# Performance work log

Measured on AMD Instinct MI355X. Metric: run time of the kernel, lower is better.

## Reference

```python
import jax, jax.numpy as jnp
import numpy as np
from jax import lax

BN_EPS = 1e-5
HEADS = 2


def dw_conv(x, w, stride, pad):
    # depthwise conv, NCHW, weight OIHW with I=1, groups=C
    return lax.conv_general_dilated(
        x, w, (stride, stride), [(pad, pad), (pad, pad)],
        dimension_numbers=('NCHW', 'OIHW', 'NCHW'),
        feature_group_count=x.shape[1])


def bn(x, g, b, m, v):
    inv = g * lax.rsqrt(v + BN_EPS)
    return (x - m[:, None, None]) * inv[:, None, None] + b[:, None, None]


def conv1x1(x, w, b):
    return jnp.einsum('bchw,oc->bohw', x, w) + b[:, None, None]


def setup_inputs() -> dict:
    key = jax.random.key(0)
    ks = jax.random.split(key, 20)
    B, C, H, W = 32, 128, 56, 56
    r = lambda i, shape, s=0.05: jax.random.normal(ks[i], shape, jnp.float32) * s
    return {
        'x': jax.random.normal(ks[0], (B, C, H, W), jnp.float32),
        'q_w': r(1, (C, C)), 'q_b': r(2, (C,)),
        'kv_w': r(3, (2 * C, C)), 'kv_b': r(4, (2 * C,)),
        'sr1_w': r(5, (C, 1, 4, 4), 0.2),
        'sr1_g': jax.random.uniform(ks[6], (C,), jnp.float32) + 0.5,
        'sr1_b': r(7, (C,)),
        'sr1_m': r(8, (C,)),
        'sr1_v': jax.random.uniform(ks[9], (C,), jnp.float32) + 0.5,
        'sr2_w': r(10, (C, 1, 1, 1), 0.5),
        'sr2_g': jax.random.uniform(ks[11], (C,), jnp.float32) + 0.5,
        'sr2_b': r(12, (C,)),
        'sr2_m': r(13, (C,)),
        'sr2_v': jax.random.uniform(ks[14], (C,), jnp.float32) + 0.5,
        'local_w': r(15, (C, 1, 3, 3), 0.2), 'local_b': r(16, (C,)),
    }


def reference(x, q_w, q_b, kv_w, kv_b,
              sr1_w, sr1_g, sr1_b, sr1_m, sr1_v,
              sr2_w, sr2_g, sr2_b, sr2_m, sr2_v,
              local_w, local_b):
    B, C, H, W = x.shape
    h = HEADS
    d = C // h
    scale = d ** -0.5

    # q projection: 1x1 conv -> [B, h, N, d]
    q = conv1x1(x, q_w, q_b)
    q = q.reshape(B, h, d, H * W).transpose(0, 1, 3, 2)

    # spatial reduction: depthwise strided conv + BN + ReLU, then depthwise 1x1 + BN
    kv = jax.nn.relu(bn(dw_conv(x, sr1_w, 4, 2), sr1_g, sr1_b, sr1_m, sr1_v))
    kv = bn(kv * sr2_w.reshape(C, 1, 1), sr2_g, sr2_b, sr2_m, sr2_v)

    # depthwise 3x3 local conv + residual
    kv = dw_conv(kv, local_w, 1, 1) + local_b[:, None, None] + kv

    # kv projection and split
    kvp = conv1x1(kv, kv_w, kv_b)
    k, v = jnp.split(kvp, 2, axis=1)
    Nk = k.shape[2] * k.shape[3]
    k = k.reshape(B, h, d, Nk)                       # [B,h,d,Nk]
    v = v.reshape(B, h, d, Nk).transpose(0, 1, 3, 2)  # [B,h,Nk,d]

    attn = jax.nn.softmax(jnp.einsum('bhnd,bhdm->bhnm', q, k) * scale, axis=-1)
    out = jnp.einsum('bhnm,bhmd->bhnd', attn, v)      # [B,h,N,d]
    return out.transpose(0, 1, 3, 2).reshape(B, C, H, W)
```

## Files before the change

### kernel.cpp

```cpp
#include <hip/hip_runtime.h>
#include <hip/hip_bf16.h>

#define B_    32
#define C_    128
#define H_    56
#define W_    56
#define N_    3136
#define HK_   15
#define NK_   225
#define D_    64
#define SCL_  0.1803368801111731f

typedef __attribute__((ext_vector_type(8))) short bf16x8;
typedef __attribute__((ext_vector_type(4))) float f32x4;

__device__ __forceinline__ float b2f(unsigned short u) {
    union { float f; unsigned int i; } x;
    x.i = ((unsigned int)u) << 16;
    return x.f;
}
__device__ __forceinline__ unsigned short f2b(float f) {
    __hip_bfloat16 h = __float2bfloat16(f);
    return *(unsigned short*)&h;
}
__device__ __forceinline__ unsigned int cvtpk(float a, float b) {
    unsigned int r;
    asm("v_cvt_pk_bf16_f32 %0, %1, %2" : "=v"(r) : "v"(a), "v"(b));
    return r;
}
__device__ __forceinline__ float exp2a(float x) {
    float r;
    asm("v_exp_f32 %0, %1" : "=v"(r) : "v"(x));
    return r;
}

__device__ __forceinline__ void gll16(const char* g, char* l) {
    __builtin_amdgcn_global_load_lds(
        (const __attribute__((address_space(1))) unsigned int*)g,
        (__attribute__((address_space(3))) unsigned int*)l,
        16, 0, 0);
}

__global__ __launch_bounds__(256) void prep_kernel(
        const float* __restrict__ x,
        const float* __restrict__ sr1_w, const float* __restrict__ sr1_g,
        const float* __restrict__ sr1_b, const float* __restrict__ sr1_m,
        const float* __restrict__ sr1_v, const float* __restrict__ sr2_w,
        const float* __restrict__ sr2_g, const float* __restrict__ sr2_b,
        const float* __restrict__ sr2_m, const float* __restrict__ sr2_v,
        const float* __restrict__ local_w, const float* __restrict__ local_b,
        const float* __restrict__ q_w, const float* __restrict__ q_b,
        const float* __restrict__ kv_w, const float* __restrict__ kv_b,
        float* __restrict__ kv2,
        unsigned short* __restrict__ wkq_sw, unsigned short* __restrict__ wv_sw,
        float* __restrict__ kwb, float* __restrict__ wb, float* __restrict__ qkb) {
    int tid = threadIdx.x;
    __shared__ float kvt[HK_][HK_ + 1];
    __shared__ float wq[64][16];

    if (blockIdx.x >= (unsigned)(B_ * C_)) {
        int bx = blockIdx.x - B_ * C_;
        int h  = bx >> 3, cg = bx & 7;
        for (int idx = tid; idx < 64 * 16; idx += 256)
            wq[idx >> 4][idx & 15] =
                q_w[(size_t)(h * 64 + (idx >> 4)) * 128 + cg * 16 + (idx & 15)];
        __syncthreads();
        {
            int cl = tid >> 4;
            int c  = cg * 16 + cl;
            int cp0 = (tid & 15) * 8;
            float acc[8];
#pragma unroll
            for (int i = 0; i < 8; ++i) acc[i] = 0.f;
            for (int e = 0; e < 64; ++e) {
                float wqv = wq[e][cl];
                const float* wkrow = kv_w + (size_t)(h * 64 + e) * 128 + cp0;
#pragma unroll
                for (int i = 0; i < 8; ++i) acc[i] += wqv * wkrow[i];
            }
            char* base = (char*)wkq_sw + (size_t)h * 32768 + (size_t)c * 256;
            ushort4 u0, u1;
            u0.x = f2b(acc[0] * SCL_); u0.y = f2b(acc[1] * SCL_);
            u0.z = f2b(acc[2] * SCL_); u0.w = f2b(acc[3] * SCL_);
            u1.x = f2b(acc[4] * SCL_); u1.y = f2b(acc[5] * SCL_);
            u1.z = f2b(acc[6] * SCL_); u1.w = f2b(acc[7] * SCL_);
            int sw = (c & 7) << 4;
            *(ushort4*)(base + ((cp0 * 2) ^ sw)) = u0;
            *(ushort4*)(base + ((cp0 * 2 + 8) ^ sw)) = u1;
        }
        if (tid < 16) {
            int cl = tid, c = cg * 16 + cl;
            float s = 0.f;
            for (int e = 0; e < 64; ++e) s += kv_b[h * 64 + e] * wq[e][cl];
            kwb[h * 128 + c] = s * SCL_;
        }
        if (cg == 0) {
            if (tid < 128) {
                float s = 0.f;
                for (int e = 0; e < 64; ++e)
                    s += q_b[h * 64 + e] * kv_w[(size_t)(h * 64 + e) * 128 + tid];
                wb[h * 128 + tid] = s * SCL_;
            }
            if (tid == 0) {
                float s = 0.f;
                for (int e = 0; e < 64; ++e) s += q_b[h * 64 + e] * kv_b[h * 64 + e];
                qkb[h] = s * SCL_;
            }
        }
        if (cg == 1) {
            for (int idx = tid; idx < 64 * 128; idx += 256) {
                int e = idx >> 7, cp = idx & 127;
                unsigned short val = f2b(kv_w[(size_t)(128 + h * 64 + e) * 128 + cp]);
                *(unsigned short*)((char*)wv_sw + (size_t)h * 16384 + (size_t)e * 256 +
                                   (((cp * 2) ^ ((e & 7) << 4)))) = val;
            }
        }
        return;
    }

    int bc = blockIdx.x;
    int c  = bc & (C_ - 1);
    const float* xp = x + (size_t)bc * (H_ * W_);
    int p = tid;
    int oy = p / HK_, ox = p % HK_;
    if (p < NK_) {
        float s = 0.f;
#pragma unroll
        for (int ky = 0; ky < 4; ++ky) {
            int iy = oy * 4 - 2 + ky;
            if (iy < 0 || iy >= H_) continue;
#pragma unroll
            for (int kx = 0; kx < 4; ++kx) {
                int ix = ox * 4 - 2 + kx;
                if (ix < 0 || ix >= W_) continue;
                s += xp[iy * W_ + ix] * sr1_w[c * 16 + ky * 4 + kx];
            }
        }
        float inv1 = sr1_g[c] * rsqrtf(sr1_v[c] + 1e-5f);
        s = (s - sr1_m[c]) * inv1 + sr1_b[c];
        s = fmaxf(s, 0.f);
        s *= sr2_w[c];
        float inv2 = sr2_g[c] * rsqrtf(sr2_v[c] + 1e-5f);
        s = (s - sr2_m[c]) * inv2 + sr2_b[c];
        kvt[oy][ox] = s;
    }
    __syncthreads();
    if (p < NK_) {
        float v = kvt[oy][ox] + local_b[c];
#pragma unroll
        for (int dy = -1; dy <= 1; ++dy) {
            int yy = oy + dy;
            if (yy < 0 || yy >= HK_) continue;
#pragma unroll
            for (int dx = -1; dx <= 1; ++dx) {
                int xx = ox + dx;
                if (xx < 0 || xx >= HK_) continue;
                v += kvt[yy][xx] * local_w[c * 9 + (dy + 1) * 3 + (dx + 1)];
            }
        }
        kv2[(size_t)bc * NK_ + p] = v;
    }
}

#define L2B(r, cb) ((r) * 256 + ((cb) ^ (((r) & 7) << 4)))
__global__ __launch_bounds__(256, 2) void kvw_kernel(
        const float* __restrict__ kv2,
        const float* __restrict__ kv_b,
        const unsigned short* __restrict__ wkq_sw,
        const unsigned short* __restrict__ wv_sw,
        const float* __restrict__ kwb,
        const float* __restrict__ wb,
        const float* __restrict__ qkb,
        unsigned short* __restrict__ kw,
        float* __restrict__ bias_s,
        unsigned short* __restrict__ vbuf) {
    int b = blockIdx.x, h = blockIdx.y, mh = blockIdx.z;
    int bh = b * 2 + h;
    int m0 = mh * 64;
    int tid = threadIdx.x;
    int lo = tid & 15, hi = (tid >> 4) & 3, wid = tid >> 6;

    __shared__ char K2[16384];
    __shared__ char WQ[32768];
    __shared__ char WV[16384];

    {
        const char* srcQ = (const char*)wkq_sw + (size_t)h * 32768 + tid * 16;
        char* dstQ = WQ + wid * 1024;
#pragma unroll
        for (int i = 0; i < 8; ++i) gll16(srcQ + i * 4096, dstQ + i * 4096);
        const char* srcV = (const char*)wv_sw + (size_t)h * 16384 + tid * 16;
        char* dstV = WV + wid * 1024;
#pragma unroll
        for (int i = 0; i < 4; ++i) gll16(srcV + i * 4096, dstV + i * 4096);
    }
    {
        int j = tid & 63;
        int mg = m0 + j;
        bool val = (mg < NK_);
#pragma unroll
        for (int it = 0; it < 8; ++it) {
            int c0 = (tid >> 6) * 4 + it * 16;
            ushort4 u;
            if (val) {
                const float* kp = kv2 + ((size_t)b * 128 + c0) * NK_ + mg;
                u.x = f2b(kp[0]);
                u.y = f2b(kp[NK_]);
                u.z = f2b(kp[2 * NK_]);
                u.w = f2b(kp[3 * NK_]);
            } else { u.x = 0; u.y = 0; u.z = 0; u.w = 0; }
            *(ushort4*)(K2 + L2B(j, c0 * 2)) = u;
        }
    }
    __syncthreads();

    bf16x8 aq[4];
#pragma unroll
    for (int ks = 0; ks < 4; ++ks)
        aq[ks] = *(const bf16x8*)(K2 + L2B(wid * 16 + lo, ks * 64 + hi * 16));

    char* kwB = (char*)kw + (size_t)bh * 65536;
#pragma unroll
    for (int ct = 0; ct < 8; ++ct) {
        f32x4 acc = {0.f, 0.f, 0.f, 0.f};
#pragma unroll
        for (int ks = 0; ks < 4; ++ks) {
            bf16x8 bq = *(const bf16x8*)(WQ + L2B(ct * 16 + lo, ks * 64 + hi * 16));
            acc = __builtin_amdgcn_mfma_f32_16x16x32_bf16(aq[ks], bq, acc, 0, 0, 0);
        }
        int c = ct * 16 + lo;
        float kb = kwb[h * 128 + c];
#pragma unroll
        for (int r = 0; r < 4; ++r) {
            int mg = m0 + wid * 16 + hi * 4 + r;
            *(unsigned short*)(kwB + (size_t)mg * 256 + (((c * 2) ^ ((mg & 7) << 4)))) =
                f2b(acc[r] + kb);
        }
    }

    char* vB = (char*)vbuf + (size_t)bh * 32768;
#pragma unroll
    for (int et = 0; et < 4; ++et) {
        f32x4 acc = {0.f, 0.f, 0.f, 0.f};
#pragma unroll
        for (int ks = 0; ks < 4; ++ks) {
            bf16x8 bv = *(const bf16x8*)(WV + L2B(et * 16 + lo, ks * 64 + hi * 16));
            acc = __builtin_amdgcn_mfma_f32_16x16x32_bf16(aq[ks], bv, acc, 0, 0, 0);
        }
        int e = et * 16 + lo;
        float vb = kv_b[128 + h * 64 + e];
#pragma unroll
        for (int r = 0; r < 4; ++r) {
            int mg = m0 + wid * 16 + hi * 4 + r;
            *(unsigned short*)(vB + (size_t)e * 512 + (((mg * 2) ^ ((e & 7) << 4)))) =
                f2b(acc[r] + vb);
        }
    }

    if (tid < 64) {
        int mg = m0 + tid;
        float s;
        if (mg >= NK_) s = -1e30f;
        else {
            s = qkb[h];
            for (int i = 0; i < 128; ++i) {
                int cp = (i + (tid & 7) * 16) & 127;
                s += b2f(*(const unsigned short*)(K2 + L2B(tid, cp * 2))) * wb[h * 128 + cp];
            }
        }
        bias_s[(size_t)bh * 256 + mg] = s;
    }
}

#define KWB(rl, cb) ((rl) * 256 + ((cb) ^ (((rl) & 7) << 4)))
#define CVB(e, cb)  ((e) * 512 + ((cb) ^ (((e) & 7) << 4)))

__global__ __launch_bounds__(256, 3) void attn_kernel(
        const float* __restrict__ x,
        const unsigned short* __restrict__ kw,
        const float* __restrict__ bias_s,
        const unsigned short* __restrict__ vbuf,
        float* __restrict__ out) {
    int flat = blockIdx.x;
    int xcd  = flat & 7;
    int idx  = flat >> 3;
    int g    = idx / 49;
    int jt   = idx % 49;
    int bh   = g * 8 + xcd;
    int bb   = bh >> 1;
    int h    = bh & 1;
    int n0   = jt * 64;
    int tid = threadIdx.x;
    int lo  = tid & 15;
    int hi  = (tid >> 4) & 3;
    int wid = tid >> 6;
    int jw  = wid * 16;

    __shared__ char LA[16384];
    __shared__ char LC[32768];
    __shared__ float LBIAS[256];

    const char* kwG = (const char*)kw + (size_t)bh * 65536;
    const char* vG  = (const char*)vbuf + (size_t)bh * 32768;

    const float* xb = x + ((size_t)bb * 128) * N_ + n0 + jw + lo;
    float xf[4][8];
#pragma unroll
    for (int ks = 0; ks < 4; ++ks) {
#pragma unroll
        for (int i = 0; i < 8; ++i)
            xf[ks][i] = xb[(size_t)(ks * 32 + hi * 8 + i) * N_];
    }
    __builtin_amdgcn_sched_barrier(0);

    {
        if (wid == 0)
            gll16((const char*)(bias_s + (size_t)bh * 256) + tid * 16, (char*)LBIAS);
        const char* s0 = kwG + tid * 16;
        char* d0 = LA + wid * 1024;
        gll16(s0, d0); gll16(s0 + 4096, d0 + 4096);
        const char* s1 = kwG + 8192 + tid * 16;
        char* d1 = LA + 8192 + wid * 1024;
        gll16(s1, d1); gll16(s1 + 4096, d1 + 4096);
        const char* sc = vG + tid * 16;
        char* dc = LC + wid * 1024;
#pragma unroll
        for (int i = 0; i < 8; ++i) gll16(sc + i * 4096, dc + i * 4096);
    }

    bf16x8 aq[4];
#pragma unroll
    for (int ks = 0; ks < 4; ++ks) {
        uint4 u;
        u.x = cvtpk(xf[ks][0], xf[ks][1]);
        u.y = cvtpk(xf[ks][2], xf[ks][3]);
        u.z = cvtpk(xf[ks][4], xf[ks][5]);
        u.w = cvtpk(xf[ks][6], xf[ks][7]);
        aq[ks] = *(bf16x8*)&u;
    }

    asm volatile("s_waitcnt vmcnt(10)" ::: "memory");
    __builtin_amdgcn_s_barrier();
    __builtin_amdgcn_sched_barrier(0);

    f32x4 s[15];
#pragma unroll
    for (int t = 0; t < 8; ++t) {
        char* Bt = LA + (t & 1) * 8192;
        __builtin_amdgcn_s_setprio(1);
#pragma unroll
        for (int ml = 0; ml < 2; ++ml) {
            int mt = t * 2 + ml;
            if (mt >= 15) continue;
            f32x4 acc = *(const f32x4*)&LBIAS[mt * 16 + hi * 4];
#pragma unroll
            for (int ks = 0; ks < 4; ++ks) {
                bf16x8 bk = *(const bf16x8*)(Bt + KWB(ml * 16 + lo, ks * 64 + hi * 16));
                acc = __builtin_amdgcn_mfma_f32_16x16x32_bf16(bk, aq[ks], acc, 0, 0, 0);
            }
            s[mt] = acc;
        }
        __builtin_amdgcn_s_setprio(0);
        if (t < 6) {
            __builtin_amdgcn_s_barrier();
            const char* sn = kwG + (t + 2) * 8192 + tid * 16;
            char* dn = LA + (t & 1) * 8192 + wid * 1024;
            gll16(sn, dn); gll16(sn + 4096, dn + 4096);
        }
        if (t < 7) {
            if (t == 0)      asm volatile("s_waitcnt vmcnt(10)" ::: "memory");
            else if (t < 6)  asm volatile("s_waitcnt vmcnt(2)" ::: "memory");
            else             asm volatile("s_waitcnt vmcnt(0)" ::: "memory");
            __builtin_amdgcn_s_barrier();
            __builtin_amdgcn_sched_barrier(0);
        }
    }

    float smv = 0.f;
#pragma unroll
    for (int mt = 0; mt < 15; ++mt) {
#pragma unroll
        for (int r = 0; r < 4; ++r) {
            float pe = exp2a(fminf(s[mt][r], 30.f));
            s[mt][r] = pe;
            smv += pe;
        }
    }
    smv += __shfl_xor(smv, 16);
    smv += __shfl_xor(smv, 32);
    float rinv = 1.f / smv;

    bf16x8 bp[8];
    int sA = lo + (hi & 1) * 32;
    int sB = sA + 16;
    bool lowm = (hi < 2);
#pragma unroll
    for (int ks = 0; ks < 8; ++ks) {
        int t0 = 2 * ks, t1 = 2 * ks + 1;
        unsigned int a0 = cvtpk(s[t0][0], s[t0][1]);
        unsigned int a1 = cvtpk(s[t0][2], s[t0][3]);
        unsigned int r0A = (unsigned int)__shfl((int)a0, sA);
        unsigned int r1A = (unsigned int)__shfl((int)a1, sA);
        unsigned int r0B = (unsigned int)__shfl((int)a0, sB);
        unsigned int r1B = (unsigned int)__shfl((int)a1, sB);
        unsigned int dw0, dw1, dw2, dw3;
        if (ks < 7) {
            unsigned int b0 = cvtpk(s[t1][0], s[t1][1]);
            unsigned int b1 = cvtpk(s[t1][2], s[t1][3]);
            unsigned int q0A = (unsigned int)__shfl((int)b0, sA);
            unsigned int q1A = (unsigned int)__shfl((int)b1, sA);
            unsigned int q0B = (unsigned int)__shfl((int)b0, sB);
            unsigned int q1B = (unsigned int)__shfl((int)b1, sB);
            dw0 = lowm ? r0A : q0A;
            dw1 = lowm ? r1A : q1A;
            dw2 = lowm ? r0B : q0B;
            dw3 = lowm ? r1B : q1B;
        } else {
            dw0 = lowm ? r0A : 0u;
            dw1 = lowm ? r1A : 0u;
            dw2 = lowm ? r0B : 0u;
            dw3 = lowm ? r1B : 0u;
        }
        uint4 d4 = {dw0, dw1, dw2, dw3};
        bp[ks] = *(bf16x8*)&d4;
    }

#pragma unroll
    for (int et = 0; et < 4; ++et) {
        f32x4 acc = {0.f, 0.f, 0.f, 0.f};
        __builtin_amdgcn_s_setprio(1);
#pragma unroll
        for (int ks = 0; ks < 8; ++ks) {
            bf16x8 av = *(const bf16x8*)(LC + CVB(et * 16 + lo, ks * 64 + hi * 16));
            acc = __builtin_amdgcn_mfma_f32_16x16x32_bf16(av, bp[ks], acc, 0, 0, 0);
        }
        __builtin_amdgcn_s_setprio(0);
        int e = et * 16 + hi * 4;
#pragma unroll
        for (int r = 0; r < 4; ++r)
            out[((size_t)bb * 128 + h * 64 + e + r) * N_ + n0 + jw + lo] = acc[r] * rinv;
    }
}

extern "C" void kernel_launch(void* const* d_in, const int* in_sizes, int n_in,
                              void* d_out, int out_size, void* d_ws, size_t ws_size,
                              hipStream_t stream) {
    const float* x       = (const float*)d_in[0];
    const float* q_w     = (const float*)d_in[1];
    const float* q_b     = (const float*)d_in[2];
    const float* kv_w    = (const float*)d_in[3];
    const float* kv_b    = (const float*)d_in[4];
    const float* sr1_w   = (const float*)d_in[5];
    const float* sr1_g   = (const float*)d_in[6];
    const float* sr1_b   = (const float*)d_in[7];
    const float* sr1_m   = (const float*)d_in[8];
    const float* sr1_v   = (const float*)d_in[9];
    const float* sr2_w   = (const float*)d_in[10];
    const float* sr2_g   = (const float*)d_in[11];
    const float* sr2_b   = (const float*)d_in[12];
    const float* sr2_m   = (const float*)d_in[13];
    const float* sr2_v   = (const float*)d_in[14];
    const float* local_w = (const float*)d_in[15];
    const float* local_b = (const float*)d_in[16];

    char* ws = (char*)d_ws;
    float* kv2              = (float*)(ws + 0);
    unsigned short* wkq_sw  = (unsigned short*)(ws + 3686400);
    unsigned short* wv_sw   = (unsigned short*)(ws + 3751936);
    unsigned short* kw      = (unsigned short*)(ws + 3784704);
    unsigned short* vbuf    = (unsigned short*)(ws + 7979008);
    float* bias_s           = (float*)(ws + 10076160);
    float* kwb              = (float*)(ws + 10141696);
    float* wb               = (float*)(ws + 10142720);
    float* qkb              = (float*)(ws + 10143744);

    prep_kernel<<<B_ * C_ + 16, 256, 0, stream>>>(
        x, sr1_w, sr1_g, sr1_b, sr1_m, sr1_v,
        sr2_w, sr2_g, sr2_b, sr2_m, sr2_v, local_w, local_b,
        q_w, q_b, kv_w, kv_b,
        kv2, wkq_sw, wv_sw, kwb, wb, qkb);
    kvw_kernel<<<dim3(B_, 2, 4), 256, 0, stream>>>(
        kv2, kv_b, wkq_sw, wv_sw, kwb, wb, qkb, kw, bias_s, vbuf);
    attn_kernel<<<3136, 256, 0, stream>>>(
        x, kw, bias_s, vbuf, (float*)d_out);
}
```

Measured before the change: 92.64 us.

## Process two query tiles per attention block to reuse staged V and bias

Each attention block now handles up to two 64-query tiles of the same batch-head, so the grid shrinks from 3136 to 1600 blocks. The V tile and softmax bias stay in LDS for the second tile, and only the K-weight stream is reloaded. The second tile's x loads and first K chunks are issued while the first tile's PV product and stores run. The s_setprio hints are dropped. The trade-off is fewer blocks with a longer serial body, an uneven last pass (ib 24 has no second tile), and possibly higher register pressure from the overlapped x prefetch.

```diff
diff --git a/kernel.cpp b/kernel.cpp
--- a/kernel.cpp
+++ b/kernel.cpp
@@ -275,6 +275,125 @@
 #define KWB(rl, cb) ((rl) * 256 + ((cb) ^ (((rl) & 7) << 4)))
 #define CVB(e, cb)  ((e) * 512 + ((cb) ^ (((e) & 7) << 4)))
 
+#define PACK_AQ(XF, AQ) do {                                                     \
+    _Pragma("unroll")                                                            \
+    for (int ks = 0; ks < 4; ++ks) {                                             \
+        uint4 u_;                                                                \
+        u_.x = cvtpk(XF[ks][0], XF[ks][1]);                                      \
+        u_.y = cvtpk(XF[ks][2], XF[ks][3]);                                      \
+        u_.z = cvtpk(XF[ks][4], XF[ks][5]);                                      \
+        u_.w = cvtpk(XF[ks][6], XF[ks][7]);                                      \
+        AQ[ks] = *(bf16x8*)&u_;                                                  \
+    }                                                                            \
+} while (0)
+
+#define ISSUE_KW01() do {                                                        \
+    const char* s0_ = kwG + tid * 16;                                            \
+    gll16(s0_, LA + wid * 1024);                                                 \
+    gll16(s0_ + 4096, LA + wid * 1024 + 4096);                                   \
+    const char* s1_ = kwG + 8192 + tid * 16;                                     \
+    gll16(s1_, LA + 8192 + wid * 1024);                                          \
+    gll16(s1_ + 4096, LA + 8192 + wid * 1024 + 4096);                            \
+} while (0)
+
+#define SLOOP(AQ, W0STR) do {                                                    \
+    _Pragma("unroll")                                                            \
+    for (int t = 0; t < 8; ++t) {                                                \
+        char* Bt_ = LA + (t & 1) * 8192;                                         \
+        _Pragma("unroll")                                                        \
+        for (int ml = 0; ml < 2; ++ml) {                                         \
+            int mt = t * 2 + ml;                                                 \
+            if (mt >= 15) continue;                                              \
+            f32x4 acc_ = *(const f32x4*)&LBIAS[mt * 16 + hi * 4];                \
+            _Pragma("unroll")                                                    \
+            for (int ks = 0; ks < 4; ++ks) {                                     \
+                bf16x8 bk_ = *(const bf16x8*)(Bt_ + KWB(ml * 16 + lo, ks * 64 + hi * 16)); \
+                acc_ = __builtin_amdgcn_mfma_f32_16x16x32_bf16(bk_, AQ[ks], acc_, 0, 0, 0); \
+            }                                                                    \
+            s[mt] = acc_;                                                        \
+        }                                                                        \
+        if (t < 6) {                                                             \
+            __builtin_amdgcn_s_barrier();                                        \
+            const char* sn_ = kwG + (t + 2) * 8192 + tid * 16;                   \
+            char* dn_ = LA + (t & 1) * 8192 + wid * 1024;                        \
+            gll16(sn_, dn_); gll16(sn_ + 4096, dn_ + 4096);                      \
+        }                                                                        \
+        if (t < 7) {                                                             \
+            if (t == 0)      asm volatile("s_waitcnt " W0STR ::: "memory");      \
+            else if (t < 6)  asm volatile("s_waitcnt vmcnt(2)" ::: "memory");    \
+            else             asm volatile("s_waitcnt vmcnt(0)" ::: "memory");    \
+            __builtin_amdgcn_s_barrier();                                        \
+            __builtin_amdgcn_sched_barrier(0);                                   \
+        }                                                                        \
+    }                                                                            \
+} while (0)
+
+#define SMTR(BP, RINV) do {                                                      \
+    float smv_ = 0.f;                                                            \
+    _Pragma("unroll")                                                            \
+    for (int mt = 0; mt < 15; ++mt) {                                            \
+        _Pragma("unroll")                                                        \
+        for (int r = 0; r < 4; ++r) {                                            \
+            float pe_ = exp2a(fminf(s[mt][r], 30.f));                            \
+            s[mt][r] = pe_;                                                      \
+            smv_ += pe_;                                                         \
+        }                                                                        \
+    }                                                                            \
+    smv_ += __shfl_xor(smv_, 16);                                                \
+    smv_ += __shfl_xor(smv_, 32);                                                \
+    RINV = 1.f / smv_;                                                           \
+    int sA_ = lo + (hi & 1) * 32;                                                \
+    int sB_ = sA_ + 16;                                                          \
+    bool lowm_ = (hi < 2);                                                       \
+    _Pragma("unroll")                                                            \
+    for (int ks = 0; ks < 8; ++ks) {                                             \
+        int t0_ = 2 * ks, t1_ = 2 * ks + 1;                                      \
+        unsigned int a0_ = cvtpk(s[t0_][0], s[t0_][1]);                          \
+        unsigned int a1_ = cvtpk(s[t0_][2], s[t0_][3]);                          \
+        unsigned int r0A_ = (unsigned int)__shfl((int)a0_, sA_);                 \
+        unsigned int r1A_ = (unsigned int)__shfl((int)a1_, sA_);                 \
+        unsigned int r0B_ = (unsigned int)__shfl((int)a0_, sB_);                 \
+        unsigned int r1B_ = (unsigned int)__shfl((int)a1_, sB_);                 \
+        unsigned int dw0_, dw1_, dw2_, dw3_;                                     \
+        if (ks < 7) {                                                            \
+            unsigned int b0_ = cvtpk(s[t1_][0], s[t1_][1]);                      \
+            unsigned int b1_ = cvtpk(s[t1_][2], s[t1_][3]);                      \
+            unsigned int q0A_ = (unsigned int)__shfl((int)b0_, sA_);             \
+            unsigned int q1A_ = (unsigned int)__shfl((int)b1_, sA_);             \
+            unsigned int q0B_ = (unsigned int)__shfl((int)b0_, sB_);             \
+            unsigned int q1B_ = (unsigned int)__shfl((int)b1_, sB_);             \
+            dw0_ = lowm_ ? r0A_ : q0A_;                                          \
+            dw1_ = lowm_ ? r1A_ : q1A_;                                          \
+            dw2_ = lowm_ ? r0B_ : q0B_;                                          \
+            dw3_ = lowm_ ? r1B_ : q1B_;                                          \
+        } else {                                                                 \
+            dw0_ = lowm_ ? r0A_ : 0u;                                            \
+            dw1_ = lowm_ ? r1A_ : 0u;                                            \
+            dw2_ = lowm_ ? r0B_ : 0u;                                            \
+            dw3_ = lowm_ ? r1B_ : 0u;                                            \
+        }                                                                        \
+        uint4 d4_ = {dw0_, dw1_, dw2_, dw3_};                                    \
+        BP[ks] = *(bf16x8*)&d4_;                                                 \
+    }                                                                            \
+} while (0)
+
+#define PVSTORE(BP, RINV, N0) do {                                               \
+    _Pragma("unroll")                                                            \
+    for (int et = 0; et < 4; ++et) {                                             \
+        f32x4 acc_ = {0.f, 0.f, 0.f, 0.f};                                       \
+        _Pragma("unroll")                                                        \
+        for (int ks = 0; ks < 8; ++ks) {                                         \
+            bf16x8 av_ = *(const bf16x8*)(LC + CVB(et * 16 + lo, ks * 64 + hi * 16)); \
+            acc_ = __builtin_amdgcn_mfma_f32_16x16x32_bf16(av_, BP[ks], acc_, 0, 0, 0); \
+        }                                                                        \
+        int e_ = et * 16 + hi * 4;                                               \
+        _Pragma("unroll")                                                        \
+        for (int r = 0; r < 4; ++r)                                              \
+            out[((size_t)bb * 128 + h * 64 + e_ + r) * N_ + (N0) + jw + lo] =    \
+                acc_[r] * (RINV);                                                \
+    }                                                                            \
+} while (0)
+
 __global__ __launch_bounds__(256, 3) void attn_kernel(
         const float* __restrict__ x,
         const unsigned short* __restrict__ kw,
@@ -284,12 +403,14 @@
     int flat = blockIdx.x;
     int xcd  = flat & 7;
     int idx  = flat >> 3;
-    int g    = idx / 49;
-    int jt   = idx % 49;
+    int g    = idx / 25;
+    int ib   = idx % 25;
     int bh   = g * 8 + xcd;
     int bb   = bh >> 1;
     int h    = bh & 1;
-    int n0   = jt * 64;
+    int n01  = ib * 64;
+    int n02  = (ib + 25) * 64;
+    bool two = (ib + 25) < 49;
     int tid = threadIdx.x;
     int lo  = tid & 15;
     int hi  = (tid >> 4) & 3;
@@ -302,143 +423,66 @@
 
     const char* kwG = (const char*)kw + (size_t)bh * 65536;
     const char* vG  = (const char*)vbuf + (size_t)bh * 32768;
-
-    const float* xb = x + ((size_t)bb * 128) * N_ + n0 + jw + lo;
+    const float* xB = x + ((size_t)bb * 128) * N_;
+
     float xf[4][8];
-#pragma unroll
-    for (int ks = 0; ks < 4; ++ks) {
-#pragma unroll
-        for (int i = 0; i < 8; ++i)
-            xf[ks][i] = xb[(size_t)(ks * 32 + hi * 8 + i) * N_];
+    {
+        const float* xb = xB + n01 + jw + lo;
+#pragma unroll
+        for (int ks = 0; ks < 4; ++ks) {
+#pragma unroll
+            for (int i = 0; i < 8; ++i)
+                xf[ks][i] = xb[(size_t)(ks * 32 + hi * 8 + i) * N_];
+        }
     }
     __builtin_amdgcn_sched_barrier(0);
 
     {
         if (wid == 0)
             gll16((const char*)(bias_s + (size_t)bh * 256) + tid * 16, (char*)LBIAS);
-        const char* s0 = kwG + tid * 16;
-        char* d0 = LA + wid * 1024;
-        gll16(s0, d0); gll16(s0 + 4096, d0 + 4096);
-        const char* s1 = kwG + 8192 + tid * 16;
-        char* d1 = LA + 8192 + wid * 1024;
-        gll16(s1, d1); gll16(s1 + 4096, d1 + 4096);
+        ISSUE_KW01();
         const char* sc = vG + tid * 16;
-        char* dc = LC + wid * 1024;
-#pragma unroll
-        for (int i = 0; i < 8; ++i) gll16(sc + i * 4096, dc + i * 4096);
+#pragma unroll
+        for (int i = 0; i < 8; ++i) gll16(sc + i * 4096, LC + i * 4096 + wid * 1024);
     }
 
     bf16x8 aq[4];
-#pragma unroll
-    for (int ks = 0; ks < 4; ++ks) {
-        uint4 u;
-        u.x = cvtpk(xf[ks][0], xf[ks][1]);
-        u.y = cvtpk(xf[ks][2], xf[ks][3]);
-        u.z = cvtpk(xf[ks][4], xf[ks][5]);
-        u.w = cvtpk(xf[ks][6], xf[ks][7]);
-        aq[ks] = *(bf16x8*)&u;
-    }
+    PACK_AQ(xf, aq);
 
     asm volatile("s_waitcnt vmcnt(10)" ::: "memory");
     __builtin_amdgcn_s_barrier();
     __builtin_amdgcn_sched_barrier(0);
 
     f32x4 s[15];
-#pragma unroll
-    for (int t = 0; t < 8; ++t) {
-        char* Bt = LA + (t & 1) * 8192;
-        __builtin_amdgcn_s_setprio(1);
-#pragma unroll
-        for (int ml = 0; ml < 2; ++ml) {
-            int mt = t * 2 + ml;
-            if (mt >= 15) continue;
-            f32x4 acc = *(const f32x4*)&LBIAS[mt * 16 + hi * 4];
-#pragma unroll
-            for (int ks = 0; ks < 4; ++ks) {
-                bf16x8 bk = *(const bf16x8*)(Bt + KWB(ml * 16 + lo, ks * 64 + hi * 16));
-                acc = __builtin_amdgcn_mfma_f32_16x16x32_bf16(bk, aq[ks], acc, 0, 0, 0);
-            }
-            s[mt] = acc;
-        }
-        __builtin_amdgcn_s_setprio(0);
-        if (t < 6) {
-            __builtin_amdgcn_s_barrier();
-            const char* sn = kwG + (t + 2) * 8192 + tid * 16;
-            char* dn = LA + (t & 1) * 8192 + wid * 1024;
-            gll16(sn, dn); gll16(sn + 4096, dn + 4096);
-        }
-        if (t < 7) {
-            if (t == 0)      asm volatile("s_waitcnt vmcnt(10)" ::: "memory");
-            else if (t < 6)  asm volatile("s_waitcnt vmcnt(2)" ::: "memory");
-            else             asm volatile("s_waitcnt vmcnt(0)" ::: "memory");
-            __builtin_amdgcn_s_barrier();
-            __builtin_amdgcn_sched_barrier(0);
-        }
-    }
-
-    float smv = 0.f;
-#pragma unroll
-    for (int mt = 0; mt < 15; ++mt) {
-#pragma unroll
-        for (int r = 0; r < 4; ++r) {
-            float pe = exp2a(fminf(s[mt][r], 30.f));
-            s[mt][r] = pe;
-            smv += pe;
-        }
-    }
-    smv += __shfl_xor(smv, 16);
-    smv += __shfl_xor(smv, 32);
-    float rinv = 1.f / smv;
-
+    SLOOP(aq, "vmcnt(10)");
+    float rinv;
     bf16x8 bp[8];
-    int sA = lo + (hi & 1) * 32;
-    int sB = sA + 16;
-    bool lowm = (hi < 2);
-#pragma unroll
-    for (int ks = 0; ks < 8; ++ks) {
-        int t0 = 2 * ks, t1 = 2 * ks + 1;
-        unsigned int a0 = cvtpk(s[t0][0], s[t0][1]);
-        unsigned int a1 = cvtpk(s[t0][2], s[t0][3]);
-        unsigned int r0A = (unsigned int)__shfl((int)a0, sA);
-        unsigned int r1A = (unsigned int)__shfl((int)a1, sA);
-        unsigned int r0B = (unsigned int)__shfl((int)a0, sB);
-        unsigned int r1B = (unsigned int)__shfl((int)a1, sB);
-        unsigned int dw0, dw1, dw2, dw3;
-        if (ks < 7) {
-            unsigned int b0 = cvtpk(s[t1][0], s[t1][1]);
-            unsigned int b1 = cvtpk(s[t1][2], s[t1][3]);
-            unsigned int q0A = (unsigned int)__shfl((int)b0, sA);
-            unsigned int q1A = (unsigned int)__shfl((int)b1, sA);
-            unsigned int q0B = (unsigned int)__shfl((int)b0, sB);
-            unsigned int q1B = (unsigned int)__shfl((int)b1, sB);
-            dw0 = lowm ? r0A : q0A;
-            dw1 = lowm ? r1A : q1A;
-            dw2 = lowm ? r0B : q0B;
-            dw3 = lowm ? r1B : q1B;
-        } else {
-            dw0 = lowm ? r0A : 0u;
-            dw1 = lowm ? r1A : 0u;
-            dw2 = lowm ? r0B : 0u;
-            dw3 = lowm ? r1B : 0u;
-        }
-        uint4 d4 = {dw0, dw1, dw2, dw3};
-        bp[ks] = *(bf16x8*)&d4;
-    }
-
-#pragma unroll
-    for (int et = 0; et < 4; ++et) {
-        f32x4 acc = {0.f, 0.f, 0.f, 0.f};
-        __builtin_amdgcn_s_setprio(1);
-#pragma unroll
-        for (int ks = 0; ks < 8; ++ks) {
-            bf16x8 av = *(const bf16x8*)(LC + CVB(et * 16 + lo, ks * 64 + hi * 16));
-            acc = __builtin_amdgcn_mfma_f32_16x16x32_bf16(av, bp[ks], acc, 0, 0, 0);
-        }
-        __builtin_amdgcn_s_setprio(0);
-        int e = et * 16 + hi * 4;
-#pragma unroll
-        for (int r = 0; r < 4; ++r)
-            out[((size_t)bb * 128 + h * 64 + e + r) * N_ + n0 + jw + lo] = acc[r] * rinv;
+    SMTR(bp, rinv);
+
+    if (two) {
+        const float* xb = xB + n02 + jw + lo;
+#pragma unroll
+        for (int ks = 0; ks < 4; ++ks) {
+#pragma unroll
+            for (int i = 0; i < 8; ++i)
+                xf[ks][i] = xb[(size_t)(ks * 32 + hi * 8 + i) * N_];
+        }
+    }
+    __builtin_amdgcn_s_barrier();
+    if (two) {
+        ISSUE_KW01();
+    }
+
+    PVSTORE(bp, rinv, n01);
+
+    if (two) {
+        PACK_AQ(xf, aq);
+        asm volatile("s_waitcnt vmcnt(2)" ::: "memory");
+        __builtin_amdgcn_s_barrier();
+        __builtin_amdgcn_sched_barrier(0);
+        SLOOP(aq, "vmcnt(2)");
+        SMTR(bp, rinv);
+        PVSTORE(bp, rinv, n02);
     }
 }
 
@@ -481,6 +525,6 @@
         kv2, wkq_sw, wv_sw, kwb, wb, qkb);
     kvw_kernel<<<dim3(B_, 2, 4), 256, 0, stream>>>(
         kv2, kv_b, wkq_sw, wv_sw, kwb, wb, qkb, kw, bias_s, vbuf);
-    attn_kernel<<<3136, 256, 0, stream>>>(
+    attn_kernel<<<1600, 256, 0, stream>>>(
         x, kw, bias_s, vbuf, (float*)d_out);
 }
```

New measurement: 96.17 us. 1.04x slower.

## Load K operand directly from global into registers instead of staging in LDS

Applied to the files above, without the earlier changes.

The attention kernel no longer double-buffers the projected K tiles through shared memory with async global-to-LDS copies and per-tile barriers. Each lane now reads its K fragments straight from global memory (L2) into registers, with a two-slot register ping-pong that prefetches the next tile. The K buffer is written without the XOR swizzle, since it is no longer read from LDS. This cuts LDS use and removes most barriers, which should raise occupancy, but every wave now issues redundant global loads of the same K data and depends on L2 latency being hidden.

```diff
diff --git a/kernel.cpp b/kernel.cpp
--- a/kernel.cpp
+++ b/kernel.cpp
@@ -233,8 +233,7 @@
 #pragma unroll
         for (int r = 0; r < 4; ++r) {
             int mg = m0 + wid * 16 + hi * 4 + r;
-            *(unsigned short*)(kwB + (size_t)mg * 256 + (((c * 2) ^ ((mg & 7) << 4)))) =
-                f2b(acc[r] + kb);
+            *(unsigned short*)(kwB + (size_t)mg * 256 + c * 2) = f2b(acc[r] + kb);
         }
     }
 
@@ -272,7 +271,6 @@
     }
 }
 
-#define KWB(rl, cb) ((rl) * 256 + ((cb) ^ (((rl) & 7) << 4)))
 #define CVB(e, cb)  ((e) * 512 + ((cb) ^ (((e) & 7) << 4)))
 
 __global__ __launch_bounds__(256, 3) void attn_kernel(
@@ -296,7 +294,6 @@
     int wid = tid >> 6;
     int jw  = wid * 16;
 
-    __shared__ char LA[16384];
     __shared__ char LC[32768];
     __shared__ float LBIAS[256];
 
@@ -316,12 +313,6 @@
     {
         if (wid == 0)
             gll16((const char*)(bias_s + (size_t)bh * 256) + tid * 16, (char*)LBIAS);
-        const char* s0 = kwG + tid * 16;
-        char* d0 = LA + wid * 1024;
-        gll16(s0, d0); gll16(s0 + 4096, d0 + 4096);
-        const char* s1 = kwG + 8192 + tid * 16;
-        char* d1 = LA + 8192 + wid * 1024;
-        gll16(s1, d1); gll16(s1 + 4096, d1 + 4096);
         const char* sc = vG + tid * 16;
         char* dc = LC + wid * 1024;
 #pragma unroll
@@ -339,41 +330,39 @@
         aq[ks] = *(bf16x8*)&u;
     }
 
-    asm volatile("s_waitcnt vmcnt(10)" ::: "memory");
+    asm volatile("s_waitcnt vmcnt(8)" ::: "memory");
     __builtin_amdgcn_s_barrier();
-    __builtin_amdgcn_sched_barrier(0);
-
+
+    const char* kwR = kwG + (size_t)lo * 256 + hi * 16;
     f32x4 s[15];
-#pragma unroll
-    for (int t = 0; t < 8; ++t) {
-        char* Bt = LA + (t & 1) * 8192;
-        __builtin_amdgcn_s_setprio(1);
-#pragma unroll
-        for (int ml = 0; ml < 2; ++ml) {
-            int mt = t * 2 + ml;
-            if (mt >= 15) continue;
-            f32x4 acc = *(const f32x4*)&LBIAS[mt * 16 + hi * 4];
-#pragma unroll
-            for (int ks = 0; ks < 4; ++ks) {
-                bf16x8 bk = *(const bf16x8*)(Bt + KWB(ml * 16 + lo, ks * 64 + hi * 16));
-                acc = __builtin_amdgcn_mfma_f32_16x16x32_bf16(bk, aq[ks], acc, 0, 0, 0);
-            }
-            s[mt] = acc;
-        }
-        __builtin_amdgcn_s_setprio(0);
-        if (t < 6) {
-            __builtin_amdgcn_s_barrier();
-            const char* sn = kwG + (t + 2) * 8192 + tid * 16;
-            char* dn = LA + (t & 1) * 8192 + wid * 1024;
-            gll16(sn, dn); gll16(sn + 4096, dn + 4096);
-        }
-        if (t < 7) {
-            if (t == 0)      asm volatile("s_waitcnt vmcnt(10)" ::: "memory");
-            else if (t < 6)  asm volatile("s_waitcnt vmcnt(2)" ::: "memory");
-            else             asm volatile("s_waitcnt vmcnt(0)" ::: "memory");
-            __builtin_amdgcn_s_barrier();
-            __builtin_amdgcn_sched_barrier(0);
-        }
+    bf16x8 cA[4], cB[4];
+#pragma unroll
+    for (int ks = 0; ks < 4; ++ks)
+        cA[ks] = *(const bf16x8*)(kwR + ks * 64);
+#pragma unroll
+    for (int mt = 0; mt < 15; ++mt) {
+        if (mt + 1 < 15) {
+            if ((mt & 1) == 0) {
+#pragma unroll
+                for (int ks = 0; ks < 4; ++ks)
+                    cB[ks] = *(const bf16x8*)(kwR + (size_t)(mt + 1) * 4096 + ks * 64);
+            } else {
+#pragma unroll
+                for (int ks = 0; ks < 4; ++ks)
+                    cA[ks] = *(const bf16x8*)(kwR + (size_t)(mt + 1) * 4096 + ks * 64);
+            }
+        }
+        f32x4 acc = *(const f32x4*)&LBIAS[mt * 16 + hi * 4];
+        if ((mt & 1) == 0) {
+#pragma unroll
+            for (int ks = 0; ks < 4; ++ks)
+                acc = __builtin_amdgcn_mfma_f32_16x16x32_bf16(cA[ks], aq[ks], acc, 0, 0, 0);
+        } else {
+#pragma unroll
+            for (int ks = 0; ks < 4; ++ks)
+                acc = __builtin_amdgcn_mfma_f32_16x16x32_bf16(cB[ks], aq[ks], acc, 0, 0, 0);
+        }
+        s[mt] = acc;
     }
 
     float smv = 0.f;
@@ -425,16 +414,17 @@
         bp[ks] = *(bf16x8*)&d4;
     }
 
+    asm volatile("s_waitcnt vmcnt(0)" ::: "memory");
+    __builtin_amdgcn_s_barrier();
+
 #pragma unroll
     for (int et = 0; et < 4; ++et) {
         f32x4 acc = {0.f, 0.f, 0.f, 0.f};
-        __builtin_amdgcn_s_setprio(1);
 #pragma unroll
         for (int ks = 0; ks < 8; ++ks) {
             bf16x8 av = *(const bf16x8*)(LC + CVB(et * 16 + lo, ks * 64 + hi * 16));
             acc = __builtin_amdgcn_mfma_f32_16x16x32_bf16(av, bp[ks], acc, 0, 0, 0);
         }
-        __builtin_amdgcn_s_setprio(0);
         int e = et * 16 + hi * 4;
 #pragma unroll
         for (int r = 0; r < 4; ++r)
```

Result: slower. 145.4 us (+57.0%).

## Pre-transpose x to bf16 token-major layout and add max-subtracted softmax

Applied to the files above, without the earlier changes.

Adds a kernel that converts x to bf16 in [B,N,C] layout, so the attention kernel loads its Q operand with 16-byte vector loads instead of strided fp32 scalar loads plus conversion. It is only used when the workspace is large enough. The change also drops the setprio hints around the MFMA loops and replaces the clamped exp with a max-subtracted softmax for numerical safety. The cost is an extra kernel launch and roughly 25 MB of extra write and read traffic.

```diff
diff --git a/kernel.cpp b/kernel.cpp
--- a/kernel.cpp
+++ b/kernel.cpp
@@ -159,6 +159,34 @@
             }
         }
         kv2[(size_t)bc * NK_ + p] = v;
+    }
+}
+
+__global__ __launch_bounds__(256) void xprep_kernel(
+        const float* __restrict__ x, unsigned short* __restrict__ xT) {
+    int nt = blockIdx.x;
+    int bb = blockIdx.y;
+    int n0 = nt * 64;
+    int tid = threadIdx.x;
+    __shared__ unsigned short T[64][132];
+
+    const float* xp = x + (size_t)bb * 128 * N_ + n0;
+#pragma unroll
+    for (int it = 0; it < 32; ++it) {
+        int c = it * 4 + (tid >> 6);
+        int j = tid & 63;
+        T[j][c] = f2b(xp[(size_t)c * N_ + j]);
+    }
+    __syncthreads();
+    unsigned short* op = xT + ((size_t)bb * N_ + n0) * 128;
+#pragma unroll
+    for (int it = 0; it < 4; ++it) {
+        int idx = it * 256 + tid;
+        int j = idx >> 4, c0 = (idx & 15) * 8;
+        ushort4 a = *(const ushort4*)&T[j][c0];
+        ushort4 b = *(const ushort4*)&T[j][c0 + 4];
+        *(ushort4*)&op[(size_t)j * 128 + c0]     = a;
+        *(ushort4*)&op[(size_t)j * 128 + c0 + 4] = b;
     }
 }
 
@@ -275,8 +303,10 @@
 #define KWB(rl, cb) ((rl) * 256 + ((cb) ^ (((rl) & 7) << 4)))
 #define CVB(e, cb)  ((e) * 512 + ((cb) ^ (((e) & 7) << 4)))
 
+template<int USE_XT>
 __global__ __launch_bounds__(256, 3) void attn_kernel(
         const float* __restrict__ x,
+        const unsigned short* __restrict__ xT,
         const unsigned short* __restrict__ kw,
         const float* __restrict__ bias_s,
         const unsigned short* __restrict__ vbuf,
@@ -303,13 +333,21 @@
     const char* kwG = (const char*)kw + (size_t)bh * 65536;
     const char* vG  = (const char*)vbuf + (size_t)bh * 32768;
 
-    const float* xb = x + ((size_t)bb * 128) * N_ + n0 + jw + lo;
+    bf16x8 aq[4];
     float xf[4][8];
-#pragma unroll
-    for (int ks = 0; ks < 4; ++ks) {
-#pragma unroll
-        for (int i = 0; i < 8; ++i)
-            xf[ks][i] = xb[(size_t)(ks * 32 + hi * 8 + i) * N_];
+    if (USE_XT) {
+        const unsigned short* xTb = xT + ((size_t)bb * N_ + n0 + jw + lo) * 128;
+#pragma unroll
+        for (int ks = 0; ks < 4; ++ks)
+            aq[ks] = *(const bf16x8*)(xTb + ks * 32 + hi * 8);
+    } else {
+        const float* xb = x + ((size_t)bb * 128) * N_ + n0 + jw + lo;
+#pragma unroll
+        for (int ks = 0; ks < 4; ++ks) {
+#pragma unroll
+            for (int i = 0; i < 8; ++i)
+                xf[ks][i] = xb[(size_t)(ks * 32 + hi * 8 + i) * N_];
+        }
     }
     __builtin_amdgcn_sched_barrier(0);
 
@@ -328,15 +366,16 @@
         for (int i = 0; i < 8; ++i) gll16(sc + i * 4096, dc + i * 4096);
     }
 
-    bf16x8 aq[4];
-#pragma unroll
-    for (int ks = 0; ks < 4; ++ks) {
-        uint4 u;
-        u.x = cvtpk(xf[ks][0], xf[ks][1]);
-        u.y = cvtpk(xf[ks][2], xf[ks][3]);
-        u.z = cvtpk(xf[ks][4], xf[ks][5]);
-        u.w = cvtpk(xf[ks][6], xf[ks][7]);
-        aq[ks] = *(bf16x8*)&u;
+    if (!USE_XT) {
+#pragma unroll
+        for (int ks = 0; ks < 4; ++ks) {
+            uint4 u;
+            u.x = cvtpk(xf[ks][0], xf[ks][1]);
+            u.y = cvtpk(xf[ks][2], xf[ks][3]);
+            u.z = cvtpk(xf[ks][4], xf[ks][5]);
+            u.w = cvtpk(xf[ks][6], xf[ks][7]);
+            aq[ks] = *(bf16x8*)&u;
+        }
     }
 
     asm volatile("s_waitcnt vmcnt(10)" ::: "memory");
@@ -347,7 +386,6 @@
 #pragma unroll
     for (int t = 0; t < 8; ++t) {
         char* Bt = LA + (t & 1) * 8192;
-        __builtin_amdgcn_s_setprio(1);
 #pragma unroll
         for (int ml = 0; ml < 2; ++ml) {
             int mt = t * 2 + ml;
@@ -360,7 +398,6 @@
             }
             s[mt] = acc;
         }
-        __builtin_amdgcn_s_setprio(0);
         if (t < 6) {
             __builtin_amdgcn_s_barrier();
             const char* sn = kwG + (t + 2) * 8192 + tid * 16;
@@ -376,12 +413,20 @@
         }
     }
 
+    float mxv = fmaxf(fmaxf(s[0][0], s[0][1]), fmaxf(s[0][2], s[0][3]));
+#pragma unroll
+    for (int mt = 1; mt < 15; ++mt) {
+        float a = fmaxf(fmaxf(s[mt][0], s[mt][1]), fmaxf(s[mt][2], s[mt][3]));
+        mxv = fmaxf(mxv, a);
+    }
+    mxv = fmaxf(mxv, __shfl_xor(mxv, 16));
+    mxv = fmaxf(mxv, __shfl_xor(mxv, 32));
     float smv = 0.f;
 #pragma unroll
     for (int mt = 0; mt < 15; ++mt) {
 #pragma unroll
         for (int r = 0; r < 4; ++r) {
-            float pe = exp2a(fminf(s[mt][r], 30.f));
+            float pe = exp2a(s[mt][r] - mxv);
             s[mt][r] = pe;
             smv += pe;
         }
@@ -428,13 +473,11 @@
 #pragma unroll
     for (int et = 0; et < 4; ++et) {
         f32x4 acc = {0.f, 0.f, 0.f, 0.f};
-        __builtin_amdgcn_s_setprio(1);
 #pragma unroll
         for (int ks = 0; ks < 8; ++ks) {
             bf16x8 av = *(const bf16x8*)(LC + CVB(et * 16 + lo, ks * 64 + hi * 16));
             acc = __builtin_amdgcn_mfma_f32_16x16x32_bf16(av, bp[ks], acc, 0, 0, 0);
         }
-        __builtin_amdgcn_s_setprio(0);
         int e = et * 16 + hi * 4;
 #pragma unroll
         for (int r = 0; r < 4; ++r)
@@ -473,14 +516,22 @@
     float* kwb              = (float*)(ws + 10141696);
     float* wb               = (float*)(ws + 10142720);
     float* qkb              = (float*)(ws + 10143744);
+    unsigned short* xT      = (unsigned short*)(ws + 10144000);
+    const size_t NEED_XT    = 10144000ULL + 25690112ULL;
+
+    bool useXT = (ws_size >= NEED_XT);
 
     prep_kernel<<<B_ * C_ + 16, 256, 0, stream>>>(
         x, sr1_w, sr1_g, sr1_b, sr1_m, sr1_v,
         sr2_w, sr2_g, sr2_b, sr2_m, sr2_v, local_w, local_b,
         q_w, q_b, kv_w, kv_b,
         kv2, wkq_sw, wv_sw, kwb, wb, qkb);
+    if (useXT)
+        xprep_kernel<<<dim3(49, B_), 256, 0, stream>>>(x, xT);
     kvw_kernel<<<dim3(B_, 2, 4), 256, 0, stream>>>(
         kv2, kv_b, wkq_sw, wv_sw, kwb, wb, qkb, kw, bias_s, vbuf);
-    attn_kernel<<<3136, 256, 0, stream>>>(
-        x, kw, bias_s, vbuf, (float*)d_out);
-}
+    if (useXT)
+        attn_kernel<1><<<3136, 256, 0, stream>>>(x, xT, kw, bias_s, vbuf, (float*)d_out);
+    else
+        attn_kernel<0><<<3136, 256, 0, stream>>>(x, xT, kw, bias_s, vbuf, (float*)d_out);
+}
```

New measurement: 96.96 us. +4.7%, slower.
